# Kernel optimization log

Hardware: AMD Instinct MI355X
Metric: run time of the kernel (lower is better)

Reference implementation:

```python
import jax, jax.numpy as jnp
import numpy as np

N, D, R = 32768, 64, 32
EPS = 1e-12


def setup_inputs() -> dict:
    key = jax.random.key(0)
    k1, k2, k3, k4 = jax.random.split(key, 4)
    Xz = jax.random.normal(k1, (N, D), dtype=jnp.float32)
    centers = jax.random.normal(k2, (R, D), dtype=jnp.float32)
    # positive rule widths in [0.5, 1.5)
    sigmas = jax.random.uniform(k3, (R, D), dtype=jnp.float32) + 0.5
    theta = jax.random.normal(k4, (R, D + 1), dtype=jnp.float32)
    return {"Xz": Xz, "centers": centers, "sigmas": sigmas, "theta": theta}


def reference(Xz, centers, sigmas, theta):
    n, d = Xz.shape
    r = centers.shape[0]
    # per-rule Gaussian log-membership: (N, R)
    z = (Xz[:, None, :] - centers[None, :, :]) / (sigmas[None, :, :] + EPS)
    log_w = -0.5 * jnp.sum(z * z, axis=-1)
    # softmax-style normalization with the original's epsilon in the denominator
    w = jnp.exp(log_w - jnp.max(log_w, axis=1, keepdims=True))
    w = w / (jnp.sum(w, axis=1, keepdims=True) + EPS)  # (N, R)
    # design matrix: for each rule r, [w_r, w_r * x] -> (N, R*(1+D))
    X1 = jnp.concatenate([jnp.ones((n, 1), dtype=Xz.dtype), Xz], axis=1)  # (N, 1+D)
    Phi = (w[:, :, None] * X1[:, None, :]).reshape(n, r * (d + 1))
    y = Phi @ theta.reshape(-1)  # (N,)
    return y[:, None], w, Phi
```

## Files before the change

kernel.cpp:

```cpp
#include <hip/hip_runtime.h>


constexpr int N_ROWS = 32768;
constexpr int D = 64;
constexpr int R = 32;
constexpr float EPS = 1e-12f;
constexpr int ROWS_PER_BLOCK = 8;
constexpr int BLOCK = 256;
constexpr int PHI_COLS = R * (D + 1);
constexpr int CSTR = 68;
constexpr int XSTR = 72;

typedef float f32x4 __attribute__((ext_vector_type(4)));

__global__ __launch_bounds__(BLOCK) void tsk_kernel(
    const float* __restrict__ Xz,
    const float* __restrict__ centers,
    const float* __restrict__ sigmas,
    const float* __restrict__ theta,
    float* __restrict__ y_out,
    float* __restrict__ w_out,
    float* __restrict__ phi_out)
{
    __shared__ __align__(16) float c_lds[R][CSTR];
    __shared__ __align__(16) float is_lds[R][CSTR];
    __shared__ __align__(16) float th_lds[R][CSTR];
    __shared__ float th0_lds[R];
    __shared__ __align__(16) float x1_lds[ROWS_PER_BLOCK][XSTR];
    __shared__ float w_lds[ROWS_PER_BLOCK][R + 1];

    const int tid = threadIdx.x;
    const int row0 = blockIdx.x * ROWS_PER_BLOCK;

    for (int i = tid; i < R * D; i += BLOCK) {
        int r = i >> 6, d = i & 63;
        c_lds[r][d] = centers[i];
        is_lds[r][d] = 1.0f / (sigmas[i] + EPS);
        th_lds[r][d] = theta[r * (D + 1) + d + 1];
    }
    if (tid < R) th0_lds[tid] = theta[tid * (D + 1)];

    if (tid < 128) {
        const f32x4* x4 = (const f32x4*)(Xz + (size_t)row0 * D);
        f32x4 v = x4[tid];
        int e = 4 * tid;
        int rr = e >> 6, cc = (e & 63) + 4;
        *(f32x4*)&x1_lds[rr][cc] = v;
    }
    if (tid < ROWS_PER_BLOCK) x1_lds[tid][3] = 1.0f;
    __syncthreads();

    const int lrow = tid >> 5;
    const int r = tid & 31;
    float acc = 0.0f;
    float tdot = th0_lds[r];
#pragma unroll
    for (int q = 0; q < D / 4; ++q) {
        f32x4 cv = *(const f32x4*)&c_lds[r][4 * q];
        f32x4 iv = *(const f32x4*)&is_lds[r][4 * q];
        f32x4 tv = *(const f32x4*)&th_lds[r][4 * q];
        f32x4 xv = *(const f32x4*)&x1_lds[lrow][4 + 4 * q];
#pragma unroll
        for (int j = 0; j < 4; ++j) {
            float z = (xv[j] - cv[j]) * iv[j];
            acc = fmaf(z, z, acc);
            tdot = fmaf(tv[j], xv[j], tdot);
        }
    }
    float logw = -0.5f * acc;

    float m = logw;
#pragma unroll
    for (int off = 16; off >= 1; off >>= 1)
        m = fmaxf(m, __shfl_xor(m, off, 32));
    float ex = __expf(logw - m);
    float s = ex;
#pragma unroll
    for (int off = 16; off >= 1; off >>= 1)
        s += __shfl_xor(s, off, 32);
    float w = ex / (s + EPS);
    w_lds[lrow][r] = w;
    __builtin_nontemporal_store(w, w_out + (size_t)(row0 + lrow) * R + r);

    float yc = w * tdot;
#pragma unroll
    for (int off = 16; off >= 1; off >>= 1)
        yc += __shfl_xor(yc, off, 32);
    if (r == 0) __builtin_nontemporal_store(yc, y_out + row0 + lrow);
    __syncthreads();

    for (int k = tid; k < PHI_COLS / 4; k += BLOCK) {
        int e = 4 * k;
        int r0 = (e + 0) / 65, j0 = (e + 0) - r0 * 65;
        int r1 = (e + 1) / 65, j1 = (e + 1) - r1 * 65;
        int r2 = (e + 2) / 65, j2 = (e + 2) - r2 * 65;
        int r3 = (e + 3) / 65, j3 = (e + 3) - r3 * 65;
#pragma unroll
        for (int row = 0; row < ROWS_PER_BLOCK; ++row) {
            f32x4 o;
            o.x = w_lds[row][r0] * x1_lds[row][3 + j0];
            o.y = w_lds[row][r1] * x1_lds[row][3 + j1];
            o.z = w_lds[row][r2] * x1_lds[row][3 + j2];
            o.w = w_lds[row][r3] * x1_lds[row][3 + j3];
            f32x4* dst = (f32x4*)(phi_out + (size_t)(row0 + row) * PHI_COLS) + k;
            __builtin_nontemporal_store(o, dst);
        }
    }
}

extern "C" void kernel_launch(void* const* d_in, const int* in_sizes, int n_in,
                              void* d_out, int out_size, void* d_ws, size_t ws_size,
                              hipStream_t stream) {
    const float* Xz      = (const float*)d_in[0];
    const float* centers = (const float*)d_in[1];
    const float* sigmas  = (const float*)d_in[2];
    const float* theta   = (const float*)d_in[3];

    float* out = (float*)d_out;
    float* y_out   = out;
    float* w_out   = out + N_ROWS;
    float* phi_out = out + N_ROWS + (size_t)N_ROWS * R;

    dim3 grid(N_ROWS / ROWS_PER_BLOCK);
    tsk_kernel<<<grid, BLOCK, 0, stream>>>(Xz, centers, sigmas, theta,
                                           y_out, w_out, phi_out);
}
```

Before: 294.5 us.

## Process 16 rows per block and write Phi via lane-broadcast scalar stores

Doubles rows per block, so each half-wave computes two rows' memberships at once, and stores centers, inverse sigmas and theta in a q-major LDS layout. The Phi write no longer goes through shared memory and per-element division by 65. Each wave broadcasts weights with readlane and writes scalar stores where lanes map to feature columns. The intent is to drop the second barrier and the index arithmetic. The cost is scalar, unaligned (stride-65) stores in place of the 16-byte nontemporal vector stores, which may hurt write coalescing on this store-bound output.

```diff
diff --git a/kernel.cpp b/kernel.cpp
--- a/kernel.cpp
+++ b/kernel.cpp
@@ -5,13 +5,16 @@
 constexpr int D = 64;
 constexpr int R = 32;
 constexpr float EPS = 1e-12f;
-constexpr int ROWS_PER_BLOCK = 8;
+constexpr int ROWS_PER_BLOCK = 16;
 constexpr int BLOCK = 256;
 constexpr int PHI_COLS = R * (D + 1);
-constexpr int CSTR = 68;
-constexpr int XSTR = 72;
+constexpr int NQ = D / 4;
 
 typedef float f32x4 __attribute__((ext_vector_type(4)));
+
+__device__ __forceinline__ float readlane_f(float v, int lane) {
+    return __int_as_float(__builtin_amdgcn_readlane(__float_as_int(v), lane));
+}
 
 __global__ __launch_bounds__(BLOCK) void tsk_kernel(
     const float* __restrict__ Xz,
@@ -22,88 +25,112 @@
     float* __restrict__ w_out,
     float* __restrict__ phi_out)
 {
-    __shared__ __align__(16) float c_lds[R][CSTR];
-    __shared__ __align__(16) float is_lds[R][CSTR];
-    __shared__ __align__(16) float th_lds[R][CSTR];
-    __shared__ float th0_lds[R];
-    __shared__ __align__(16) float x1_lds[ROWS_PER_BLOCK][XSTR];
-    __shared__ float w_lds[ROWS_PER_BLOCK][R + 1];
+    __shared__ __align__(16) float cq[NQ][R][4];
+    __shared__ __align__(16) float isq[NQ][R][4];
+    __shared__ __align__(16) float thq[NQ][R][4];
+    __shared__ float th0[R];
+    __shared__ __align__(16) float x_lds[ROWS_PER_BLOCK][68];
 
-    const int tid = threadIdx.x;
+    const int tid  = threadIdx.x;
+    const int wv   = tid >> 6;
+    const int lane = tid & 63;
+    const int h    = lane >> 5;
+    const int r    = lane & 31;
     const int row0 = blockIdx.x * ROWS_PER_BLOCK;
 
     for (int i = tid; i < R * D; i += BLOCK) {
-        int r = i >> 6, d = i & 63;
-        c_lds[r][d] = centers[i];
-        is_lds[r][d] = 1.0f / (sigmas[i] + EPS);
-        th_lds[r][d] = theta[r * (D + 1) + d + 1];
+        int q = i >> 7;
+        int rem = i & 127;
+        int rr = rem >> 2, j = rem & 3;
+        int src = rr * D + (q << 2) + j;
+        ((float*)cq)[i]  = centers[src];
+        ((float*)isq)[i] = 1.0f / (sigmas[src] + EPS);
+        ((float*)thq)[i] = theta[rr * (D + 1) + 1 + (q << 2) + j];
     }
-    if (tid < R) th0_lds[tid] = theta[tid * (D + 1)];
+    if (tid < R) th0[tid] = theta[tid * (D + 1)];
 
-    if (tid < 128) {
+    {
         const f32x4* x4 = (const f32x4*)(Xz + (size_t)row0 * D);
         f32x4 v = x4[tid];
-        int e = 4 * tid;
-        int rr = e >> 6, cc = (e & 63) + 4;
-        *(f32x4*)&x1_lds[rr][cc] = v;
+        int rr = tid >> 4;
+        int cc = (4 * tid) & 63;
+        *(f32x4*)&x_lds[rr][cc] = v;
     }
-    if (tid < ROWS_PER_BLOCK) x1_lds[tid][3] = 1.0f;
     __syncthreads();
 
-    const int lrow = tid >> 5;
-    const int r = tid & 31;
-    float acc = 0.0f;
-    float tdot = th0_lds[r];
+    const int ra = 4 * wv + 2 * h;
+    float acc_a = 0.0f, acc_b = 0.0f;
+    float td_a = th0[r];
+    float td_b = td_a;
 #pragma unroll
-    for (int q = 0; q < D / 4; ++q) {
-        f32x4 cv = *(const f32x4*)&c_lds[r][4 * q];
-        f32x4 iv = *(const f32x4*)&is_lds[r][4 * q];
-        f32x4 tv = *(const f32x4*)&th_lds[r][4 * q];
-        f32x4 xv = *(const f32x4*)&x1_lds[lrow][4 + 4 * q];
+    for (int q = 0; q < NQ; ++q) {
+        f32x4 cv = *(const f32x4*)&cq[q][r][0];
+        f32x4 iv = *(const f32x4*)&isq[q][r][0];
+        f32x4 tv = *(const f32x4*)&thq[q][r][0];
+        f32x4 xa = *(const f32x4*)&x_lds[ra][4 * q];
+        f32x4 xb = *(const f32x4*)&x_lds[ra + 1][4 * q];
 #pragma unroll
         for (int j = 0; j < 4; ++j) {
-            float z = (xv[j] - cv[j]) * iv[j];
-            acc = fmaf(z, z, acc);
-            tdot = fmaf(tv[j], xv[j], tdot);
+            float za = (xa[j] - cv[j]) * iv[j];
+            float zb = (xb[j] - cv[j]) * iv[j];
+            acc_a = fmaf(za, za, acc_a);
+            acc_b = fmaf(zb, zb, acc_b);
+            td_a = fmaf(tv[j], xa[j], td_a);
+            td_b = fmaf(tv[j], xb[j], td_b);
         }
     }
-    float logw = -0.5f * acc;
+    float la = -0.5f * acc_a, lb = -0.5f * acc_b;
 
-    float m = logw;
+    float ma = la, mb = lb;
 #pragma unroll
-    for (int off = 16; off >= 1; off >>= 1)
-        m = fmaxf(m, __shfl_xor(m, off, 32));
-    float ex = __expf(logw - m);
-    float s = ex;
+    for (int off = 16; off >= 1; off >>= 1) {
+        ma = fmaxf(ma, __shfl_xor(ma, off, 32));
+        mb = fmaxf(mb, __shfl_xor(mb, off, 32));
+    }
+    float ea = __expf(la - ma), eb = __expf(lb - mb);
+    float sa = ea, sb = eb;
 #pragma unroll
-    for (int off = 16; off >= 1; off >>= 1)
-        s += __shfl_xor(s, off, 32);
-    float w = ex / (s + EPS);
-    w_lds[lrow][r] = w;
-    __builtin_nontemporal_store(w, w_out + (size_t)(row0 + lrow) * R + r);
+    for (int off = 16; off >= 1; off >>= 1) {
+        sa += __shfl_xor(sa, off, 32);
+        sb += __shfl_xor(sb, off, 32);
+    }
+    float wa = ea / (sa + EPS);
+    float wb = eb / (sb + EPS);
 
-    float yc = w * tdot;
+    w_out[(size_t)(row0 + ra) * R + r]     = wa;
+    w_out[(size_t)(row0 + ra + 1) * R + r] = wb;
+
+    float ya = wa * td_a, yb = wb * td_b;
 #pragma unroll
-    for (int off = 16; off >= 1; off >>= 1)
-        yc += __shfl_xor(yc, off, 32);
-    if (r == 0) __builtin_nontemporal_store(yc, y_out + row0 + lrow);
-    __syncthreads();
+    for (int off = 16; off >= 1; off >>= 1) {
+        ya += __shfl_xor(ya, off, 32);
+        yb += __shfl_xor(yb, off, 32);
+    }
+    if (r == 0) {
+        y_out[row0 + ra]     = ya;
+        y_out[row0 + ra + 1] = yb;
+    }
 
-    for (int k = tid; k < PHI_COLS / 4; k += BLOCK) {
-        int e = 4 * k;
-        int r0 = (e + 0) / 65, j0 = (e + 0) - r0 * 65;
-        int r1 = (e + 1) / 65, j1 = (e + 1) - r1 * 65;
-        int r2 = (e + 2) / 65, j2 = (e + 2) - r2 * 65;
-        int r3 = (e + 3) / 65, j3 = (e + 3) - r3 * 65;
+
+    {
+        float* p0 = phi_out + (size_t)(row0 + ra) * PHI_COLS + r * 65;
+        float* p1 = phi_out + (size_t)(row0 + ra + 1) * PHI_COLS + r * 65;
+        *p0 = wa;
+        *p1 = wb;
+    }
+    float xr[4];
 #pragma unroll
-        for (int row = 0; row < ROWS_PER_BLOCK; ++row) {
-            f32x4 o;
-            o.x = w_lds[row][r0] * x1_lds[row][3 + j0];
-            o.y = w_lds[row][r1] * x1_lds[row][3 + j1];
-            o.z = w_lds[row][r2] * x1_lds[row][3 + j2];
-            o.w = w_lds[row][r3] * x1_lds[row][3 + j3];
-            f32x4* dst = (f32x4*)(phi_out + (size_t)(row0 + row) * PHI_COLS) + k;
-            __builtin_nontemporal_store(o, dst);
+    for (int rr = 0; rr < 4; ++rr)
+        xr[rr] = x_lds[4 * wv + rr][lane];
+#pragma unroll
+    for (int rr = 0; rr < 4; ++rr) {
+        float* prow = phi_out + (size_t)(row0 + 4 * wv + rr) * PHI_COLS + 1 + lane;
+        const float xv = xr[rr];
+        const int srclane = (rr >> 1) * 32;
+#pragma unroll
+        for (int rl = 0; rl < R; ++rl) {
+            float ws = readlane_f((rr & 1) ? wb : wa, srclane + rl);
+            prow[rl * 65] = ws * xv;
         }
     }
 }
```

New measurement: 375.8 us. 27.6% more time.
